# Performance work log

Hardware: AMD Instinct MI355X
Metric: run time of the kernel (lower is better)

## Reference

```python
import jax, jax.numpy as jnp
import numpy as np

E, T, H, I = 8, 1024, 2048, 4096  # experts, tokens/expert, hidden, intermediate


def setup_inputs() -> dict:
    key = jax.random.key(0)
    k1, k2, k3, k4, k5 = jax.random.split(key, 5)
    x = jax.random.normal(k1, (E, T, H), dtype=jnp.float32)
    # is_transposed=True layout: [E, H, 2I] and [E, I, H]
    gate_up_proj = jax.random.normal(k2, (E, H, 2 * I), dtype=jnp.float32)
    down_proj = jax.random.normal(k3, (E, I, H), dtype=jnp.float32)
    gate_up_proj_bias = jax.random.normal(k4, (E, 2 * I), dtype=jnp.float32)
    down_proj_bias = jax.random.normal(k5, (E, H), dtype=jnp.float32)
    return {
        "x": x,
        "gate_up_proj": gate_up_proj,
        "gate_up_proj_bias": gate_up_proj_bias,
        "down_proj": down_proj,
        "down_proj_bias": down_proj_bias,
    }


def reference(x, gate_up_proj, gate_up_proj_bias, down_proj, down_proj_bias):
    # grouped GEMM: per-expert x[e] @ gate_up_proj[e] + bias  -> [E, T, 2I]
    gu = jnp.einsum("eth,eho->eto", x, gate_up_proj) + gate_up_proj_bias[:, None, :]
    gate, up = jnp.split(gu, 2, axis=-1)  # SwiGLU
    hidden = jax.nn.silu(gate) * up  # [E, T, I]
    out = jnp.einsum("eti,eih->eth", hidden, down_proj) + down_proj_bias[:, None, :]
    return out
```

## Files before the change

### kernel.cpp

```cpp
#include <hip/hip_runtime.h>


#define E_ 8
#define T_ 1024
#define H_ 2048
#define I_ 4096

typedef unsigned short ushort_t;
typedef unsigned int uint_t;
typedef float f32x4 __attribute__((ext_vector_type(4)));
typedef __bf16 bf16x8 __attribute__((ext_vector_type(8)));
typedef unsigned short ushort8 __attribute__((ext_vector_type(8)));

__device__ inline ushort_t f2bf(float f) {
  uint_t u = __float_as_uint(f);
  u += 0x7fffu + ((u >> 16) & 1u);
  return (ushort_t)(u >> 16);
}

__device__ inline void async_copy16(void* lds, const void* gptr) {
  __builtin_amdgcn_global_load_lds(
      (__attribute__((address_space(1))) void*)(void*)gptr,
      (__attribute__((address_space(3))) void*)lds,
      16, 0, 0);
}

__device__ inline int swz_kc(int chunk) {
  return ((chunk & 7) ^ ((chunk >> 3) & 7)) * 8;
}

__global__ __launch_bounds__(256) void cvt_kernel(const float* __restrict__ in,
                                                  ushort_t* __restrict__ out) {
  size_t base = (size_t)(blockIdx.x * 256 + threadIdx.x) * 8;
  f32x4 a = *(const f32x4*)(in + base);
  f32x4 b = *(const f32x4*)(in + base + 4);
  ushort8 o;
  o[0] = f2bf(a[0]); o[1] = f2bf(a[1]); o[2] = f2bf(a[2]); o[3] = f2bf(a[3]);
  o[4] = f2bf(b[0]); o[5] = f2bf(b[1]); o[6] = f2bf(b[2]); o[7] = f2bf(b[3]);
  *(ushort8*)(out + base) = o;
}

__global__ __launch_bounds__(256) void transpose_kernel(
    const float* __restrict__ in, ushort_t* __restrict__ out, int R, int C) {
  __shared__ float tile[64 * 64];
  const int e = blockIdx.z;
  const float* inb = in + (size_t)e * R * C;
  ushort_t* outb = out + (size_t)e * R * C;
  const int c0 = blockIdx.x * 64, r0 = blockIdx.y * 64;
  const int t = threadIdx.x;
  const int lrow = t >> 4, lc4 = t & 15;
#pragma unroll
  for (int rr = 0; rr < 64; rr += 16) {
    int r = lrow + rr;
    f32x4 v = *(const f32x4*)&inb[(size_t)(r0 + r) * C + c0 + lc4 * 4];
    *(f32x4*)&tile[r * 64 + 4 * (lc4 ^ (r >> 3))] = v;
  }
  __syncthreads();
  const int oc = t >> 3, orr = (t & 7) * 8;
#pragma unroll
  for (int cc = 0; cc < 64; cc += 32) {
    int c = oc + cc;
    ushort8 o;
#pragma unroll
    for (int k = 0; k < 8; ++k) {
      int r = orr + k;
      o[k] = f2bf(tile[r * 64 + 4 * ((c >> 2) ^ (r >> 3)) + (c & 3)]);
    }
    *(ushort8*)&outb[(size_t)(c0 + c) * R + r0 + orr] = o;
  }
}

#define G_BK 64

__global__ __launch_bounds__(256) void gemm1_swiglu_kernel(
    const ushort_t* __restrict__ A, const ushort_t* __restrict__ B,
    const float* __restrict__ bias, ushort_t* __restrict__ Hd) {
  __shared__ ushort_t As[128 * G_BK];
  __shared__ ushort_t Bg[64 * G_BK];
  __shared__ ushort_t Bu[64 * G_BK];
  const int e = blockIdx.z;
  const ushort_t* Ab = A + (size_t)e * T_ * H_;
  const ushort_t* Bb = B + (size_t)e * (2 * I_) * H_;
  const float* biasb = bias + (size_t)e * 2 * I_;
  const int m0 = blockIdx.y * 128;
  const int n0 = blockIdx.x * 64;
  const int tid = threadIdx.x;
  const int wv = tid >> 6, lane = tid & 63;
  const int wm = (wv >> 1) * 64, wn = (wv & 1) * 32;
  const int quad = lane >> 4, lr = lane & 15;

  f32x4 accg[4][2] = {};
  f32x4 accu[4][2] = {};

  for (int k0 = 0; k0 < H_; k0 += G_BK) {
#pragma unroll
    for (int r = 0; r < 4; ++r) {
      int chunk = r * 256 + tid;
      int row = chunk >> 3;
      async_copy16(&As[chunk * 8],
                   &Ab[(size_t)(m0 + row) * H_ + k0 + swz_kc(chunk)]);
    }
#pragma unroll
    for (int r = 0; r < 2; ++r) {
      int chunk = r * 256 + tid;
      int row = chunk >> 3;
      int kc = k0 + swz_kc(chunk);
      async_copy16(&Bg[chunk * 8], &Bb[(size_t)(n0 + row) * H_ + kc]);
      async_copy16(&Bu[chunk * 8], &Bb[(size_t)(I_ + n0 + row) * H_ + kc]);
    }
    __syncthreads();
#pragma unroll
    for (int ks = 0; ks < 2; ++ks) {
      const int sw = ((ks * 4 + quad) ^ (lr & 7)) * 8;
      bf16x8 af[4], bg[2], bu[2];
#pragma unroll
      for (int i = 0; i < 4; ++i)
        af[i] = *(const bf16x8*)&As[(wm + 16 * i + lr) * G_BK + sw];
#pragma unroll
      for (int j = 0; j < 2; ++j) {
        bg[j] = *(const bf16x8*)&Bg[(wn + 16 * j + lr) * G_BK + sw];
        bu[j] = *(const bf16x8*)&Bu[(wn + 16 * j + lr) * G_BK + sw];
      }
#pragma unroll
      for (int i = 0; i < 4; ++i)
#pragma unroll
        for (int j = 0; j < 2; ++j) {
          accg[i][j] = __builtin_amdgcn_mfma_f32_16x16x32_bf16(
              af[i], bg[j], accg[i][j], 0, 0, 0);
          accu[i][j] = __builtin_amdgcn_mfma_f32_16x16x32_bf16(
              af[i], bu[j], accu[i][j], 0, 0, 0);
        }
    }
    __syncthreads();
  }

  ushort_t* Hb = Hd + (size_t)e * T_ * I_;
#pragma unroll
  for (int j = 0; j < 2; ++j) {
    int col = n0 + wn + 16 * j + lr;
    float bgv = biasb[col];
    float buv = biasb[I_ + col];
#pragma unroll
    for (int i = 0; i < 4; ++i) {
      int rowb = m0 + wm + 16 * i + quad * 4;
#pragma unroll
      for (int r = 0; r < 4; ++r) {
        float g = accg[i][j][r] + bgv;
        float u = accu[i][j][r] + buv;
        float s = g / (1.0f + __expf(-g));
        Hb[(size_t)(rowb + r) * I_ + col] = f2bf(s * u);
      }
    }
  }
}

__global__ __launch_bounds__(256) void gemm2_kernel(
    const ushort_t* __restrict__ A, const ushort_t* __restrict__ B,
    const float* __restrict__ bias, float* __restrict__ C) {
  __shared__ ushort_t As[128 * G_BK];
  __shared__ ushort_t Bs[128 * G_BK];
  const int e = blockIdx.z;
  const ushort_t* Ab = A + (size_t)e * T_ * I_;
  const ushort_t* Bb = B + (size_t)e * H_ * I_;
  const float* biasb = bias + (size_t)e * H_;
  const int m0 = blockIdx.y * 128;
  const int n0 = blockIdx.x * 128;
  const int tid = threadIdx.x;
  const int wv = tid >> 6, lane = tid & 63;
  const int wm = (wv >> 1) * 64, wn = (wv & 1) * 64;
  const int quad = lane >> 4, lr = lane & 15;

  f32x4 acc[4][4] = {};

  for (int k0 = 0; k0 < I_; k0 += G_BK) {
#pragma unroll
    for (int r = 0; r < 4; ++r) {
      int chunk = r * 256 + tid;
      int row = chunk >> 3;
      int kc = k0 + swz_kc(chunk);
      async_copy16(&As[chunk * 8], &Ab[(size_t)(m0 + row) * I_ + kc]);
      async_copy16(&Bs[chunk * 8], &Bb[(size_t)(n0 + row) * I_ + kc]);
    }
    __syncthreads();
#pragma unroll
    for (int ks = 0; ks < 2; ++ks) {
      const int sw = ((ks * 4 + quad) ^ (lr & 7)) * 8;
      bf16x8 af[4], bfr[4];
#pragma unroll
      for (int i = 0; i < 4; ++i)
        af[i] = *(const bf16x8*)&As[(wm + 16 * i + lr) * G_BK + sw];
#pragma unroll
      for (int j = 0; j < 4; ++j)
        bfr[j] = *(const bf16x8*)&Bs[(wn + 16 * j + lr) * G_BK + sw];
#pragma unroll
      for (int i = 0; i < 4; ++i)
#pragma unroll
        for (int j = 0; j < 4; ++j)
          acc[i][j] = __builtin_amdgcn_mfma_f32_16x16x32_bf16(
              af[i], bfr[j], acc[i][j], 0, 0, 0);
    }
    __syncthreads();
  }

  float* Cb = C + (size_t)e * T_ * H_;
#pragma unroll
  for (int j = 0; j < 4; ++j) {
    int col = n0 + wn + 16 * j + lr;
    float bv = biasb[col];
#pragma unroll
    for (int i = 0; i < 4; ++i) {
      int rowb = m0 + wm + 16 * i + quad * 4;
#pragma unroll
      for (int r = 0; r < 4; ++r)
        Cb[(size_t)(rowb + r) * H_ + col] = acc[i][j][r] + bv;
    }
  }
}

extern "C" void kernel_launch(void* const* d_in, const int* in_sizes, int n_in,
                              void* d_out, int out_size, void* d_ws, size_t ws_size,
                              hipStream_t stream) {
  const float* x   = (const float*)d_in[0];
  const float* wgu = (const float*)d_in[1];
  const float* bgu = (const float*)d_in[2];
  const float* wd  = (const float*)d_in[3];
  const float* bd  = (const float*)d_in[4];
  float* out = (float*)d_out;

  char* ws = (char*)d_ws;
  ushort_t* xb     = (ushort_t*)(ws);
  ushort_t* wgu_t  = (ushort_t*)(ws + 33554432);
  ushort_t* wd_t   = (ushort_t*)(ws + 33554432 + 268435456);
  ushort_t* hidden = (ushort_t*)(ws + 33554432 + 268435456 + 134217728);

  cvt_kernel<<<8192, 256, 0, stream>>>(x, xb);
  transpose_kernel<<<dim3(2 * I_ / 64, H_ / 64, E_), 256, 0, stream>>>(
      wgu, wgu_t, H_, 2 * I_);
  transpose_kernel<<<dim3(H_ / 64, I_ / 64, E_), 256, 0, stream>>>(
      wd, wd_t, I_, H_);
  gemm1_swiglu_kernel<<<dim3(I_ / 64, T_ / 128, E_), 256, 0, stream>>>(
      xb, wgu_t, bgu, hidden);
  gemm2_kernel<<<dim3(H_ / 128, T_ / 128, E_), 256, 0, stream>>>(
      hidden, wd_t, bd, out);
}
```

Baseline: 1.511 ms.

## Rewrite both GEMMs as 256-wide, 8-wave, double-buffered pipelined kernels

Both grouped GEMMs move to larger block tiles (256x128 gate/up, 256x256 down) with 512 threads and double-buffered LDS. Global-to-LDS async loads for the next K tile are interleaved with four MFMA phases, using explicit vmcnt waits, barriers and s_setprio. The aim is to raise data reuse per LDS byte and hide global latency behind matrix math, in place of the old load-then-sync loop. In exchange each block uses 128KB of LDS, more accumulator registers and fewer blocks, which risks lower occupancy and hazards in the hand-written wait counts.

Result: faster. 1.352 ms (-10.5%).

```diff
diff --git a/kernel.cpp b/kernel.cpp
--- a/kernel.cpp
+++ b/kernel.cpp
@@ -25,8 +25,15 @@
       16, 0, 0);
 }
 
-__device__ inline int swz_kc(int chunk) {
-  return ((chunk & 7) ^ ((chunk >> 3) & 7)) * 8;
+__device__ __forceinline__ void stage_half(ushort_t* lds, const ushort_t* g,
+                                           int ld, int tid) {
+#pragma unroll
+  for (int r = 0; r < 2; ++r) {
+    int chunk = r * 512 + tid;
+    int row = chunk >> 3;
+    int kc = ((chunk & 7) ^ (row & 7)) * 8;
+    async_copy16(lds + chunk * 8, g + (size_t)row * ld + kc);
+  }
 }
 
 __global__ __launch_bounds__(256) void cvt_kernel(const float* __restrict__ in,
@@ -70,83 +77,156 @@
   }
 }
 
-#define G_BK 64
-
-__global__ __launch_bounds__(256) void gemm1_swiglu_kernel(
+#define LGKM0() asm volatile("s_waitcnt lgkmcnt(0)" ::: "memory")
+
+__global__ __launch_bounds__(512, 2) void gemm1_swiglu_kernel(
     const ushort_t* __restrict__ A, const ushort_t* __restrict__ B,
     const float* __restrict__ bias, ushort_t* __restrict__ Hd) {
-  __shared__ ushort_t As[128 * G_BK];
-  __shared__ ushort_t Bg[64 * G_BK];
-  __shared__ ushort_t Bu[64 * G_BK];
+  __shared__ ushort_t lds[2 * 32768];
+  ushort_t* bA0 = lds;
+  ushort_t* bG0 = lds + 16384;
+  ushort_t* bU0 = lds + 24576;
+  ushort_t* bA1 = lds + 32768;
+  ushort_t* bG1 = lds + 49152;
+  ushort_t* bU1 = lds + 57344;
+
   const int e = blockIdx.z;
-  const ushort_t* Ab = A + (size_t)e * T_ * H_;
-  const ushort_t* Bb = B + (size_t)e * (2 * I_) * H_;
-  const float* biasb = bias + (size_t)e * 2 * I_;
-  const int m0 = blockIdx.y * 128;
-  const int n0 = blockIdx.x * 64;
+  const int m0 = blockIdx.y * 256;
+  const int n0 = blockIdx.x * 128;
+  const ushort_t* Ab = A + (size_t)e * T_ * H_ + (size_t)m0 * H_;
+  const ushort_t* Gb = B + (size_t)e * 2 * I_ * H_ + (size_t)n0 * H_;
+  const ushort_t* Ub = B + (size_t)e * 2 * I_ * H_ + (size_t)(I_ + n0) * H_;
   const int tid = threadIdx.x;
   const int wv = tid >> 6, lane = tid & 63;
-  const int wm = (wv >> 1) * 64, wn = (wv & 1) * 32;
+  const int wm = (wv >> 2) * 128;
+  const int wn = (wv & 3) * 32;
   const int quad = lane >> 4, lr = lane & 15;
 
-  f32x4 accg[4][2] = {};
-  f32x4 accu[4][2] = {};
-
-  for (int k0 = 0; k0 < H_; k0 += G_BK) {
-#pragma unroll
-    for (int r = 0; r < 4; ++r) {
-      int chunk = r * 256 + tid;
-      int row = chunk >> 3;
-      async_copy16(&As[chunk * 8],
-                   &Ab[(size_t)(m0 + row) * H_ + k0 + swz_kc(chunk)]);
-    }
-#pragma unroll
-    for (int r = 0; r < 2; ++r) {
-      int chunk = r * 256 + tid;
-      int row = chunk >> 3;
-      int kc = k0 + swz_kc(chunk);
-      async_copy16(&Bg[chunk * 8], &Bb[(size_t)(n0 + row) * H_ + kc]);
-      async_copy16(&Bu[chunk * 8], &Bb[(size_t)(I_ + n0 + row) * H_ + kc]);
-    }
-    __syncthreads();
-#pragma unroll
-    for (int ks = 0; ks < 2; ++ks) {
-      const int sw = ((ks * 4 + quad) ^ (lr & 7)) * 8;
-      bf16x8 af[4], bg[2], bu[2];
-#pragma unroll
-      for (int i = 0; i < 4; ++i)
-        af[i] = *(const bf16x8*)&As[(wm + 16 * i + lr) * G_BK + sw];
-#pragma unroll
-      for (int j = 0; j < 2; ++j) {
-        bg[j] = *(const bf16x8*)&Bg[(wn + 16 * j + lr) * G_BK + sw];
-        bu[j] = *(const bf16x8*)&Bu[(wn + 16 * j + lr) * G_BK + sw];
-      }
-#pragma unroll
-      for (int i = 0; i < 4; ++i)
-#pragma unroll
-        for (int j = 0; j < 2; ++j) {
-          accg[i][j] = __builtin_amdgcn_mfma_f32_16x16x32_bf16(
-              af[i], bg[j], accg[i][j], 0, 0, 0);
-          accu[i][j] = __builtin_amdgcn_mfma_f32_16x16x32_bf16(
-              af[i], bu[j], accu[i][j], 0, 0, 0);
-        }
-    }
-    __syncthreads();
+  f32x4 ag[8][2] = {};
+  f32x4 au[8][2] = {};
+  bf16x8 alo[4][2], ahi[4][2], bb[2][2];
+
+  const int NT = H_ / 64;
+
+  stage_half(bA0, Ab, H_, tid);
+  stage_half(bA0 + 8192, Ab + 128 * H_, H_, tid);
+  stage_half(bG0, Gb, H_, tid);
+  stage_half(bU0, Ub, H_, tid);
+  stage_half(bA1, Ab + 64, H_, tid);
+  stage_half(bA1 + 8192, Ab + 128 * H_ + 64, H_, tid);
+  asm volatile("s_waitcnt vmcnt(4)" ::: "memory");
+  __builtin_amdgcn_s_barrier();
+  __builtin_amdgcn_sched_barrier(0);
+
+  auto tile = [&](int t, ushort_t* cA, ushort_t* cG, ushort_t* cU,
+                  ushort_t* oG, ushort_t* oU) {
+#pragma unroll
+    for (int mi = 0; mi < 4; ++mi)
+#pragma unroll
+      for (int ks = 0; ks < 2; ++ks)
+        alo[mi][ks] = *(const bf16x8*)&cA[(wm + mi * 16 + lr) * 64 +
+                                          (((ks * 4 + quad) ^ (lr & 7)) * 8)];
+#pragma unroll
+    for (int ni = 0; ni < 2; ++ni)
+#pragma unroll
+      for (int ks = 0; ks < 2; ++ks)
+        bb[ni][ks] = *(const bf16x8*)&cG[(wn + ni * 16 + lr) * 64 +
+                                         (((ks * 4 + quad) ^ (lr & 7)) * 8)];
+    if (t + 1 < NT) stage_half(oG, Gb + (size_t)(t + 1) * 64, H_, tid);
+    __builtin_amdgcn_s_barrier();
+    LGKM0();
+    __builtin_amdgcn_s_setprio(1);
+#pragma unroll
+    for (int ks = 0; ks < 2; ++ks)
+#pragma unroll
+      for (int mi = 0; mi < 4; ++mi)
+#pragma unroll
+        for (int ni = 0; ni < 2; ++ni)
+          ag[mi][ni] = __builtin_amdgcn_mfma_f32_16x16x32_bf16(
+              alo[mi][ks], bb[ni][ks], ag[mi][ni], 0, 0, 0);
+    __builtin_amdgcn_s_setprio(0);
+    __builtin_amdgcn_s_barrier();
+#pragma unroll
+    for (int mi = 0; mi < 4; ++mi)
+#pragma unroll
+      for (int ks = 0; ks < 2; ++ks)
+        ahi[mi][ks] = *(const bf16x8*)&cA[(wm + 64 + mi * 16 + lr) * 64 +
+                                          (((ks * 4 + quad) ^ (lr & 7)) * 8)];
+    if (t + 1 < NT) stage_half(oU, Ub + (size_t)(t + 1) * 64, H_, tid);
+    __builtin_amdgcn_s_barrier();
+    LGKM0();
+    __builtin_amdgcn_s_setprio(1);
+#pragma unroll
+    for (int ks = 0; ks < 2; ++ks)
+#pragma unroll
+      for (int mi = 0; mi < 4; ++mi)
+#pragma unroll
+        for (int ni = 0; ni < 2; ++ni)
+          ag[4 + mi][ni] = __builtin_amdgcn_mfma_f32_16x16x32_bf16(
+              ahi[mi][ks], bb[ni][ks], ag[4 + mi][ni], 0, 0, 0);
+    __builtin_amdgcn_s_setprio(0);
+    __builtin_amdgcn_s_barrier();
+#pragma unroll
+    for (int ni = 0; ni < 2; ++ni)
+#pragma unroll
+      for (int ks = 0; ks < 2; ++ks)
+        bb[ni][ks] = *(const bf16x8*)&cU[(wn + ni * 16 + lr) * 64 +
+                                         (((ks * 4 + quad) ^ (lr & 7)) * 8)];
+    if (t + 2 < NT) stage_half(cA, Ab + (size_t)(t + 2) * 64, H_, tid);
+    __builtin_amdgcn_s_barrier();
+    LGKM0();
+    __builtin_amdgcn_s_setprio(1);
+#pragma unroll
+    for (int ks = 0; ks < 2; ++ks)
+#pragma unroll
+      for (int mi = 0; mi < 4; ++mi)
+#pragma unroll
+        for (int ni = 0; ni < 2; ++ni)
+          au[mi][ni] = __builtin_amdgcn_mfma_f32_16x16x32_bf16(
+              alo[mi][ks], bb[ni][ks], au[mi][ni], 0, 0, 0);
+    __builtin_amdgcn_s_setprio(0);
+    __builtin_amdgcn_s_barrier();
+    if (t + 2 < NT)
+      stage_half(cA + 8192, Ab + 128 * H_ + (size_t)(t + 2) * 64, H_, tid);
+    __builtin_amdgcn_s_barrier();
+    LGKM0();
+    __builtin_amdgcn_s_setprio(1);
+#pragma unroll
+    for (int ks = 0; ks < 2; ++ks)
+#pragma unroll
+      for (int mi = 0; mi < 4; ++mi)
+#pragma unroll
+        for (int ni = 0; ni < 2; ++ni)
+          au[4 + mi][ni] = __builtin_amdgcn_mfma_f32_16x16x32_bf16(
+              ahi[mi][ks], bb[ni][ks], au[4 + mi][ni], 0, 0, 0);
+    __builtin_amdgcn_s_setprio(0);
+    if (t + 2 < NT)
+      asm volatile("s_waitcnt vmcnt(4)" ::: "memory");
+    else
+      asm volatile("s_waitcnt vmcnt(0)" ::: "memory");
+    __builtin_amdgcn_s_barrier();
+    __builtin_amdgcn_sched_barrier(0);
+  };
+
+  for (int t = 0; t < NT; t += 2) {
+    tile(t, bA0, bG0, bU0, bG1, bU1);
+    tile(t + 1, bA1, bG1, bU1, bG0, bU0);
   }
 
   ushort_t* Hb = Hd + (size_t)e * T_ * I_;
-#pragma unroll
-  for (int j = 0; j < 2; ++j) {
-    int col = n0 + wn + 16 * j + lr;
+  const float* biasb = bias + (size_t)e * 2 * I_;
+#pragma unroll
+  for (int ni = 0; ni < 2; ++ni) {
+    int col = n0 + wn + ni * 16 + lr;
     float bgv = biasb[col];
     float buv = biasb[I_ + col];
 #pragma unroll
-    for (int i = 0; i < 4; ++i) {
-      int rowb = m0 + wm + 16 * i + quad * 4;
+    for (int mi = 0; mi < 8; ++mi) {
+      int rowb = m0 + wm + mi * 16 + quad * 4;
 #pragma unroll
       for (int r = 0; r < 4; ++r) {
-        float g = accg[i][j][r] + bgv;
-        float u = accu[i][j][r] + buv;
+        float g = ag[mi][ni][r] + bgv;
+        float u = au[mi][ni][r] + buv;
         float s = g / (1.0f + __expf(-g));
         Hb[(size_t)(rowb + r) * I_ + col] = f2bf(s * u);
       }
@@ -154,65 +234,148 @@
   }
 }
 
-__global__ __launch_bounds__(256) void gemm2_kernel(
+__global__ __launch_bounds__(512, 2) void gemm2_kernel(
     const ushort_t* __restrict__ A, const ushort_t* __restrict__ B,
     const float* __restrict__ bias, float* __restrict__ C) {
-  __shared__ ushort_t As[128 * G_BK];
-  __shared__ ushort_t Bs[128 * G_BK];
+  __shared__ ushort_t lds[2 * 32768];
+  ushort_t* bA0 = lds;
+  ushort_t* bB0 = lds + 16384;
+  ushort_t* bA1 = lds + 32768;
+  ushort_t* bB1 = lds + 49152;
+
   const int e = blockIdx.z;
-  const ushort_t* Ab = A + (size_t)e * T_ * I_;
-  const ushort_t* Bb = B + (size_t)e * H_ * I_;
-  const float* biasb = bias + (size_t)e * H_;
-  const int m0 = blockIdx.y * 128;
-  const int n0 = blockIdx.x * 128;
+  const int m0 = blockIdx.y * 256;
+  const int n0 = blockIdx.x * 256;
+  const ushort_t* Ab = A + (size_t)e * T_ * I_ + (size_t)m0 * I_;
+  const ushort_t* Bb = B + (size_t)e * H_ * I_ + (size_t)n0 * I_;
   const int tid = threadIdx.x;
   const int wv = tid >> 6, lane = tid & 63;
-  const int wm = (wv >> 1) * 64, wn = (wv & 1) * 64;
+  const int wm = (wv >> 2) * 128;
+  const int wn = (wv & 3) * 64;
   const int quad = lane >> 4, lr = lane & 15;
 
-  f32x4 acc[4][4] = {};
-
-  for (int k0 = 0; k0 < I_; k0 += G_BK) {
-#pragma unroll
-    for (int r = 0; r < 4; ++r) {
-      int chunk = r * 256 + tid;
-      int row = chunk >> 3;
-      int kc = k0 + swz_kc(chunk);
-      async_copy16(&As[chunk * 8], &Ab[(size_t)(m0 + row) * I_ + kc]);
-      async_copy16(&Bs[chunk * 8], &Bb[(size_t)(n0 + row) * I_ + kc]);
-    }
-    __syncthreads();
-#pragma unroll
-    for (int ks = 0; ks < 2; ++ks) {
-      const int sw = ((ks * 4 + quad) ^ (lr & 7)) * 8;
-      bf16x8 af[4], bfr[4];
-#pragma unroll
-      for (int i = 0; i < 4; ++i)
-        af[i] = *(const bf16x8*)&As[(wm + 16 * i + lr) * G_BK + sw];
-#pragma unroll
-      for (int j = 0; j < 4; ++j)
-        bfr[j] = *(const bf16x8*)&Bs[(wn + 16 * j + lr) * G_BK + sw];
-#pragma unroll
-      for (int i = 0; i < 4; ++i)
-#pragma unroll
-        for (int j = 0; j < 4; ++j)
-          acc[i][j] = __builtin_amdgcn_mfma_f32_16x16x32_bf16(
-              af[i], bfr[j], acc[i][j], 0, 0, 0);
-    }
-    __syncthreads();
+  f32x4 acc[8][4] = {};
+  bf16x8 alo[4][2], ahi[4][2], bfr[2][2];
+
+  const int NT = I_ / 64;
+
+  stage_half(bA0, Ab, I_, tid);
+  stage_half(bA0 + 8192, Ab + 128 * I_, I_, tid);
+  stage_half(bB0, Bb, I_, tid);
+  stage_half(bB0 + 8192, Bb + 128 * I_, I_, tid);
+  stage_half(bA1, Ab + 64, I_, tid);
+  stage_half(bA1 + 8192, Ab + 128 * I_ + 64, I_, tid);
+  asm volatile("s_waitcnt vmcnt(4)" ::: "memory");
+  __builtin_amdgcn_s_barrier();
+  __builtin_amdgcn_sched_barrier(0);
+
+  auto tile = [&](int t, ushort_t* cA, ushort_t* cB, ushort_t* oB) {
+#pragma unroll
+    for (int mi = 0; mi < 4; ++mi)
+#pragma unroll
+      for (int ks = 0; ks < 2; ++ks)
+        alo[mi][ks] = *(const bf16x8*)&cA[(wm + mi * 16 + lr) * 64 +
+                                          (((ks * 4 + quad) ^ (lr & 7)) * 8)];
+#pragma unroll
+    for (int ni = 0; ni < 2; ++ni)
+#pragma unroll
+      for (int ks = 0; ks < 2; ++ks)
+        bfr[ni][ks] = *(const bf16x8*)&cB[(wn + ni * 16 + lr) * 64 +
+                                          (((ks * 4 + quad) ^ (lr & 7)) * 8)];
+    if (t + 1 < NT) stage_half(oB, Bb + (size_t)(t + 1) * 64, I_, tid);
+    __builtin_amdgcn_s_barrier();
+    LGKM0();
+    __builtin_amdgcn_s_setprio(1);
+#pragma unroll
+    for (int ks = 0; ks < 2; ++ks)
+#pragma unroll
+      for (int mi = 0; mi < 4; ++mi)
+#pragma unroll
+        for (int ni = 0; ni < 2; ++ni)
+          acc[mi][ni] = __builtin_amdgcn_mfma_f32_16x16x32_bf16(
+              alo[mi][ks], bfr[ni][ks], acc[mi][ni], 0, 0, 0);
+    __builtin_amdgcn_s_setprio(0);
+    __builtin_amdgcn_s_barrier();
+#pragma unroll
+    for (int mi = 0; mi < 4; ++mi)
+#pragma unroll
+      for (int ks = 0; ks < 2; ++ks)
+        ahi[mi][ks] = *(const bf16x8*)&cA[(wm + 64 + mi * 16 + lr) * 64 +
+                                          (((ks * 4 + quad) ^ (lr & 7)) * 8)];
+    if (t + 1 < NT)
+      stage_half(oB + 8192, Bb + 128 * I_ + (size_t)(t + 1) * 64, I_, tid);
+    __builtin_amdgcn_s_barrier();
+    LGKM0();
+    __builtin_amdgcn_s_setprio(1);
+#pragma unroll
+    for (int ks = 0; ks < 2; ++ks)
+#pragma unroll
+      for (int mi = 0; mi < 4; ++mi)
+#pragma unroll
+        for (int ni = 0; ni < 2; ++ni)
+          acc[4 + mi][ni] = __builtin_amdgcn_mfma_f32_16x16x32_bf16(
+              ahi[mi][ks], bfr[ni][ks], acc[4 + mi][ni], 0, 0, 0);
+    __builtin_amdgcn_s_setprio(0);
+    __builtin_amdgcn_s_barrier();
+#pragma unroll
+    for (int ni = 0; ni < 2; ++ni)
+#pragma unroll
+      for (int ks = 0; ks < 2; ++ks)
+        bfr[ni][ks] = *(const bf16x8*)&cB[(wn + 32 + ni * 16 + lr) * 64 +
+                                          (((ks * 4 + quad) ^ (lr & 7)) * 8)];
+    if (t + 2 < NT) stage_half(cA, Ab + (size_t)(t + 2) * 64, I_, tid);
+    __builtin_amdgcn_s_barrier();
+    LGKM0();
+    __builtin_amdgcn_s_setprio(1);
+#pragma unroll
+    for (int ks = 0; ks < 2; ++ks)
+#pragma unroll
+      for (int mi = 0; mi < 4; ++mi)
+#pragma unroll
+        for (int ni = 0; ni < 2; ++ni)
+          acc[mi][2 + ni] = __builtin_amdgcn_mfma_f32_16x16x32_bf16(
+              alo[mi][ks], bfr[ni][ks], acc[mi][2 + ni], 0, 0, 0);
+    __builtin_amdgcn_s_setprio(0);
+    __builtin_amdgcn_s_barrier();
+    if (t + 2 < NT)
+      stage_half(cA + 8192, Ab + 128 * I_ + (size_t)(t + 2) * 64, I_, tid);
+    __builtin_amdgcn_s_barrier();
+    LGKM0();
+    __builtin_amdgcn_s_setprio(1);
+#pragma unroll
+    for (int ks = 0; ks < 2; ++ks)
+#pragma unroll
+      for (int mi = 0; mi < 4; ++mi)
+#pragma unroll
+        for (int ni = 0; ni < 2; ++ni)
+          acc[4 + mi][2 + ni] = __builtin_amdgcn_mfma_f32_16x16x32_bf16(
+              ahi[mi][ks], bfr[ni][ks], acc[4 + mi][2 + ni], 0, 0, 0);
+    __builtin_amdgcn_s_setprio(0);
+    if (t + 2 < NT)
+      asm volatile("s_waitcnt vmcnt(4)" ::: "memory");
+    else
+      asm volatile("s_waitcnt vmcnt(0)" ::: "memory");
+    __builtin_amdgcn_s_barrier();
+    __builtin_amdgcn_sched_barrier(0);
+  };
+
+  for (int t = 0; t < NT; t += 2) {
+    tile(t, bA0, bB0, bB1);
+    tile(t + 1, bA1, bB1, bB0);
   }
 
   float* Cb = C + (size_t)e * T_ * H_;
-#pragma unroll
-  for (int j = 0; j < 4; ++j) {
-    int col = n0 + wn + 16 * j + lr;
+  const float* biasb = bias + (size_t)e * H_;
+#pragma unroll
+  for (int ni = 0; ni < 4; ++ni) {
+    int col = n0 + wn + ni * 16 + lr;
     float bv = biasb[col];
 #pragma unroll
-    for (int i = 0; i < 4; ++i) {
-      int rowb = m0 + wm + 16 * i + quad * 4;
+    for (int mi = 0; mi < 8; ++mi) {
+      int rowb = m0 + wm + mi * 16 + quad * 4;
 #pragma unroll
       for (int r = 0; r < 4; ++r)
-        Cb[(size_t)(rowb + r) * H_ + col] = acc[i][j][r] + bv;
+        Cb[(size_t)(rowb + r) * H_ + col] = acc[mi][ni][r] + bv;
     }
   }
 }
@@ -238,8 +401,8 @@
       wgu, wgu_t, H_, 2 * I_);
   transpose_kernel<<<dim3(H_ / 64, I_ / 64, E_), 256, 0, stream>>>(
       wd, wd_t, I_, H_);
-  gemm1_swiglu_kernel<<<dim3(I_ / 64, T_ / 128, E_), 256, 0, stream>>>(
+  gemm1_swiglu_kernel<<<dim3(I_ / 128, T_ / 256, E_), 512, 0, stream>>>(
       xb, wgu_t, bgu, hidden);
-  gemm2_kernel<<<dim3(H_ / 128, T_ / 128, E_), 256, 0, stream>>>(
+  gemm2_kernel<<<dim3(H_ / 256, T_ / 256, E_), 512, 0, stream>>>(
       hidden, wd_t, bd, out);
 }
```
